# Performance work log

Hardware: AMD Instinct MI355X
Metric: run time of the kernel (lower is better)

Reference implementation:

```python
import jax, jax.numpy as jnp
import numpy as np
import itertools

# ResamplerLayer(interpolation='LINEAR', boundary='REPLICATE'): trilinear
# resampling with replicate (clamp-to-edge) boundary handling.
# inputs: [B, X, Y, Z, C]; sample_coords: [B, D0, D1, D2, 3] in voxel units.

B, X, Y, Z, C = 2, 128, 128, 128, 4
D = 96  # output grid size per spatial dim


def setup_inputs() -> dict:
    key = jax.random.key(0)
    k1, k2 = jax.random.split(key)
    inputs = jax.random.normal(k1, (B, X, Y, Z, C), dtype=jnp.float32)
    sizes = jnp.array([X, Y, Z], dtype=jnp.float32)
    # coordinates in [-1, size] to exercise the replicate boundary slightly
    sample_coords = jax.random.uniform(k2, (B, D, D, D, 3), dtype=jnp.float32) * (sizes + 1.0) - 1.0
    return {"inputs": inputs, "sample_coords": sample_coords}


def _trilinear_replicate(inputs, sample_coords):
    spatial = inputs.shape[1:-1]          # (X, Y, Z)
    bsz = inputs.shape[0]
    floor_c = jnp.floor(sample_coords)
    w = sample_coords - floor_c           # fractional weights, [B, D0, D1, D2, 3]
    base = floor_c.astype(jnp.int32)
    # batch index broadcast against the spatial coord grid
    b_idx = jnp.arange(bsz).reshape((bsz,) + (1,) * (sample_coords.ndim - 2))
    out = jnp.zeros(sample_coords.shape[:-1] + (inputs.shape[-1],), dtype=inputs.dtype)
    for bits in itertools.product((0, 1), repeat=3):  # 8 corners (binary neighbour ids)
        ix = jnp.clip(base[..., 0] + bits[0], 0, spatial[0] - 1)  # REPLICATE boundary
        iy = jnp.clip(base[..., 1] + bits[1], 0, spatial[1] - 1)
        iz = jnp.clip(base[..., 2] + bits[2], 0, spatial[2] - 1)
        vals = inputs[b_idx, ix, iy, iz]  # gather: [B, D0, D1, D2, C]
        weight = jnp.ones(sample_coords.shape[:-1], dtype=inputs.dtype)
        for d, bit in enumerate(bits):
            weight = weight * (w[..., d] if bit else (1.0 - w[..., d]))
        out = out + vals * weight[..., None]
    return out


def reference(inputs, sample_coords):
    return _trilinear_replicate(inputs, sample_coords)
```

## Files before the change

kernel.cpp:

```cpp
#include <hip/hip_runtime.h>

#define BX 2
#define NX 128
#define NY 128
#define NZ 128
#define NC 4
#define ND 96

constexpr int PPB   = ND * ND * ND;
constexpr int TOTAL = BX * PPB;

__device__ __forceinline__ float4 f4_lerp(float4 a, float4 b, float t) {
    float4 r;
    r.x = fmaf(b.x - a.x, t, a.x);
    r.y = fmaf(b.y - a.y, t, a.y);
    r.z = fmaf(b.z - a.z, t, a.z);
    r.w = fmaf(b.w - a.w, t, a.w);
    return r;
}

__global__ __launch_bounds__(256) void ResamplerLayer_15668040696111_kernel(
    const float4* __restrict__ in,
    const float*  __restrict__ coords,
    float4*       __restrict__ out)
{
    int idx = blockIdx.x * blockDim.x + threadIdx.x;
    if (idx >= TOTAL) return;

    const float cx = coords[3 * idx + 0];
    const float cy = coords[3 * idx + 1];
    const float cz = coords[3 * idx + 2];

    const float fx = floorf(cx), fy = floorf(cy), fz = floorf(cz);
    const float wx = cx - fx, wy = cy - fy, wz = cz - fz;

    int x0 = max(0, min((int)fx,     NX - 1));
    int x1 = max(0, min((int)fx + 1, NX - 1));
    int y0 = max(0, min((int)fy,     NY - 1));
    int y1 = max(0, min((int)fy + 1, NY - 1));
    int z0 = max(0, min((int)fz,     NZ - 1));
    int z1 = max(0, min((int)fz + 1, NZ - 1));

    const int b = idx / PPB;
    const float4* __restrict__ inb = in + (size_t)b * (NX * NY * NZ);

    const float4* r00 = inb + ((size_t)x0 * NY + y0) * NZ;
    const float4* r01 = inb + ((size_t)x0 * NY + y1) * NZ;
    const float4* r10 = inb + ((size_t)x1 * NY + y0) * NZ;
    const float4* r11 = inb + ((size_t)x1 * NY + y1) * NZ;

    float4 v000 = r00[z0], v001 = r00[z1];
    float4 v010 = r01[z0], v011 = r01[z1];
    float4 v100 = r10[z0], v101 = r10[z1];
    float4 v110 = r11[z0], v111 = r11[z1];

    float4 c00 = f4_lerp(v000, v001, wz);
    float4 c01 = f4_lerp(v010, v011, wz);
    float4 c10 = f4_lerp(v100, v101, wz);
    float4 c11 = f4_lerp(v110, v111, wz);

    float4 c0 = f4_lerp(c00, c01, wy);
    float4 c1 = f4_lerp(c10, c11, wy);

    out[idx] = f4_lerp(c0, c1, wx);
}

extern "C" void kernel_launch(void* const* d_in, const int* in_sizes, int n_in,
                              void* d_out, int out_size, void* d_ws, size_t ws_size,
                              hipStream_t stream) {
    const float4* in     = (const float4*)d_in[0];
    const float*  coords = (const float*)d_in[1];
    float4*       out    = (float4*)d_out;

    const int threads = 256;
    const int blocks  = (TOTAL + threads - 1) / threads;
    ResamplerLayer_15668040696111_kernel<<<blocks, threads, 0, stream>>>(in, coords, out);
}
```

Measured before the change: 216.9 us.

## Repack input into fp16 2x2x2 bricks before trilinear gather

Adds a pre-pass that converts the input volume to half precision and reorders it into 2x2x2 voxel bricks of 64 bytes in workspace. The resample kernel then gathers its 8 corners from the brick layout, so the neighbours of one sample mostly fall in the same cache line and each voxel is half the bytes. The cost is an extra full pass over the input every call, plus fp16 rounding error in the result. A direct fp32 path is kept for when the workspace is too small.

```diff
diff --git a/kernel.cpp b/kernel.cpp
--- a/kernel.cpp
+++ b/kernel.cpp
@@ -1,14 +1,16 @@
 #include <hip/hip_runtime.h>
+#include <hip/hip_fp16.h>
 
-#define BX 2
-#define NX 128
-#define NY 128
-#define NZ 128
-#define NC 4
+#define BATCH 2
+#define NS 128
+#define NB 64
 #define ND 96
 
 constexpr int PPB   = ND * ND * ND;
-constexpr int TOTAL = BX * PPB;
+constexpr int TOTAL = BATCH * PPB;
+constexpr int BRICKS_PER_BATCH = NB * NB * NB;
+constexpr int TOTAL_BRICKS = BATCH * BRICKS_PER_BATCH;
+constexpr size_t WS_NEEDED = (size_t)TOTAL_BRICKS * 64;
 
 __device__ __forceinline__ float4 f4_lerp(float4 a, float4 b, float t) {
     float4 r;
@@ -19,7 +21,86 @@
     return r;
 }
 
-__global__ __launch_bounds__(256) void ResamplerLayer_15668040696111_kernel(
+__global__ __launch_bounds__(256) void repack_fp16_bricks(
+    const float4* __restrict__ in, uint2* __restrict__ bricks)
+{
+    int g = blockIdx.x * 256 + threadIdx.x;
+    int t = g >> 3;
+    int l = g & 7;
+    int lx = (l >> 2) & 1, ly = (l >> 1) & 1, lz = l & 1;
+    int b  = t >> 18;
+    int r  = t & 262143;
+    int x  = ((r >> 12) << 1) + lx;
+    int y  = (((r >> 6) & 63) << 1) + ly;
+    int z  = ((r & 63) << 1) + lz;
+
+    float4 v = in[(((size_t)b * NS + x) * NS + y) * NS + z];
+    __half2 h0 = __float22half2_rn(make_float2(v.x, v.y));
+    __half2 h1 = __float22half2_rn(make_float2(v.z, v.w));
+    uint2 p;
+    p.x = *(const unsigned int*)&h0;
+    p.y = *(const unsigned int*)&h1;
+    bricks[g] = p;
+}
+
+__device__ __forceinline__ float4 vox_to_f4(uint2 v) {
+    __half2 a = *(const __half2*)&v.x;
+    __half2 b = *(const __half2*)&v.y;
+    float2 f0 = __half22float2(a);
+    float2 f1 = __half22float2(b);
+    return make_float4(f0.x, f0.y, f1.x, f1.y);
+}
+
+__device__ __forceinline__ int brick_off(int x, int y, int z) {
+    int bidx = (((x >> 1) * NB) + (y >> 1)) * NB + (z >> 1);
+    return (bidx << 3) + ((x & 1) << 2) + ((y & 1) << 1) + (z & 1);
+}
+
+__global__ __launch_bounds__(256) void resample_bricks(
+    const uint2* __restrict__ bricks,
+    const float* __restrict__ coords,
+    float4*      __restrict__ out)
+{
+    int idx = blockIdx.x * 256 + threadIdx.x;
+    if (idx >= TOTAL) return;
+
+    const float cx = coords[3 * idx + 0];
+    const float cy = coords[3 * idx + 1];
+    const float cz = coords[3 * idx + 2];
+
+    const float fx = floorf(cx), fy = floorf(cy), fz = floorf(cz);
+    const float wx = cx - fx, wy = cy - fy, wz = cz - fz;
+
+    int x0 = max(0, min((int)fx,     NS - 1));
+    int x1 = max(0, min((int)fx + 1, NS - 1));
+    int y0 = max(0, min((int)fy,     NS - 1));
+    int y1 = max(0, min((int)fy + 1, NS - 1));
+    int z0 = max(0, min((int)fz,     NS - 1));
+    int z1 = max(0, min((int)fz + 1, NS - 1));
+
+    const uint2* __restrict__ wb =
+        bricks + ((idx >= PPB) ? (size_t)BRICKS_PER_BATCH * 8 : 0);
+
+    uint2 u000 = wb[brick_off(x0, y0, z0)];
+    uint2 u001 = wb[brick_off(x0, y0, z1)];
+    uint2 u010 = wb[brick_off(x0, y1, z0)];
+    uint2 u011 = wb[brick_off(x0, y1, z1)];
+    uint2 u100 = wb[brick_off(x1, y0, z0)];
+    uint2 u101 = wb[brick_off(x1, y0, z1)];
+    uint2 u110 = wb[brick_off(x1, y1, z0)];
+    uint2 u111 = wb[brick_off(x1, y1, z1)];
+
+    float4 c00 = f4_lerp(vox_to_f4(u000), vox_to_f4(u001), wz);
+    float4 c01 = f4_lerp(vox_to_f4(u010), vox_to_f4(u011), wz);
+    float4 c10 = f4_lerp(vox_to_f4(u100), vox_to_f4(u101), wz);
+    float4 c11 = f4_lerp(vox_to_f4(u110), vox_to_f4(u111), wz);
+
+    float4 c0 = f4_lerp(c00, c01, wy);
+    float4 c1 = f4_lerp(c10, c11, wy);
+    out[idx] = f4_lerp(c0, c1, wx);
+}
+
+__global__ __launch_bounds__(256) void resample_direct(
     const float4* __restrict__ in,
     const float*  __restrict__ coords,
     float4*       __restrict__ out)
@@ -30,38 +111,29 @@
     const float cx = coords[3 * idx + 0];
     const float cy = coords[3 * idx + 1];
     const float cz = coords[3 * idx + 2];
-
     const float fx = floorf(cx), fy = floorf(cy), fz = floorf(cz);
     const float wx = cx - fx, wy = cy - fy, wz = cz - fz;
 
-    int x0 = max(0, min((int)fx,     NX - 1));
-    int x1 = max(0, min((int)fx + 1, NX - 1));
-    int y0 = max(0, min((int)fy,     NY - 1));
-    int y1 = max(0, min((int)fy + 1, NY - 1));
-    int z0 = max(0, min((int)fz,     NZ - 1));
-    int z1 = max(0, min((int)fz + 1, NZ - 1));
+    int x0 = max(0, min((int)fx,     NS - 1));
+    int x1 = max(0, min((int)fx + 1, NS - 1));
+    int y0 = max(0, min((int)fy,     NS - 1));
+    int y1 = max(0, min((int)fy + 1, NS - 1));
+    int z0 = max(0, min((int)fz,     NS - 1));
+    int z1 = max(0, min((int)fz + 1, NS - 1));
 
     const int b = idx / PPB;
-    const float4* __restrict__ inb = in + (size_t)b * (NX * NY * NZ);
+    const float4* __restrict__ inb = in + (size_t)b * (NS * NS * NS);
+    const float4* r00 = inb + ((size_t)x0 * NS + y0) * NS;
+    const float4* r01 = inb + ((size_t)x0 * NS + y1) * NS;
+    const float4* r10 = inb + ((size_t)x1 * NS + y0) * NS;
+    const float4* r11 = inb + ((size_t)x1 * NS + y1) * NS;
 
-    const float4* r00 = inb + ((size_t)x0 * NY + y0) * NZ;
-    const float4* r01 = inb + ((size_t)x0 * NY + y1) * NZ;
-    const float4* r10 = inb + ((size_t)x1 * NY + y0) * NZ;
-    const float4* r11 = inb + ((size_t)x1 * NY + y1) * NZ;
-
-    float4 v000 = r00[z0], v001 = r00[z1];
-    float4 v010 = r01[z0], v011 = r01[z1];
-    float4 v100 = r10[z0], v101 = r10[z1];
-    float4 v110 = r11[z0], v111 = r11[z1];
-
-    float4 c00 = f4_lerp(v000, v001, wz);
-    float4 c01 = f4_lerp(v010, v011, wz);
-    float4 c10 = f4_lerp(v100, v101, wz);
-    float4 c11 = f4_lerp(v110, v111, wz);
-
+    float4 c00 = f4_lerp(r00[z0], r00[z1], wz);
+    float4 c01 = f4_lerp(r01[z0], r01[z1], wz);
+    float4 c10 = f4_lerp(r10[z0], r10[z1], wz);
+    float4 c11 = f4_lerp(r11[z0], r11[z1], wz);
     float4 c0 = f4_lerp(c00, c01, wy);
     float4 c1 = f4_lerp(c10, c11, wy);
-
     out[idx] = f4_lerp(c0, c1, wx);
 }
 
@@ -72,7 +144,12 @@
     const float*  coords = (const float*)d_in[1];
     float4*       out    = (float4*)d_out;
 
-    const int threads = 256;
-    const int blocks  = (TOTAL + threads - 1) / threads;
-    ResamplerLayer_15668040696111_kernel<<<blocks, threads, 0, stream>>>(in, coords, out);
+    if (ws_size >= WS_NEEDED) {
+        uint2* bricks = (uint2*)d_ws;
+        int rp_threads = TOTAL_BRICKS * 8;
+        repack_fp16_bricks<<<rp_threads / 256, 256, 0, stream>>>(in, bricks);
+        resample_bricks<<<(TOTAL + 255) / 256, 256, 0, stream>>>(bricks, coords, out);
+    } else {
+        resample_direct<<<(TOTAL + 255) / 256, 256, 0, stream>>>(in, coords, out);
+    }
 }
```

After: 195.4 us. -9.9%, faster.
